# Kernel optimization log

Measured on AMD Instinct MI355X. Metric: run time of the kernel, lower is better.

Reference implementation:

```python
import jax, jax.numpy as jnp
import numpy as np

N_EMBD = 1024
N_HEAD = 16
B, T = 2, 2048
EPS_LN = 1e-5
EPS_RENORM = 1e-8


def _layernorm(x, w, b):
    mu = jnp.mean(x, axis=-1, keepdims=True)
    var = jnp.mean(jnp.square(x - mu), axis=-1, keepdims=True)
    return (x - mu) * jax.lax.rsqrt(var + EPS_LN) * w + b


def setup_inputs() -> dict:
    key = jax.random.key(0)
    ks = jax.random.split(key, 8)
    C = N_EMBD
    s = 0.02
    return {
        "x": jax.random.normal(ks[0], (B, T, C), jnp.float32),
        "ln1_w": jnp.ones((C,), jnp.float32),
        "ln1_b": jnp.zeros((C,), jnp.float32),
        "w_attn": jax.random.normal(ks[1], (C, 3 * C), jnp.float32) * s,
        "b_attn": jnp.zeros((3 * C,), jnp.float32),
        "w_attn_proj": jax.random.normal(ks[2], (C, C), jnp.float32) * s,
        "b_attn_proj": jnp.zeros((C,), jnp.float32),
        "threshold": jnp.full((N_HEAD,), 0.01, jnp.float32),
        "leak": jnp.full((N_HEAD,), 2.0, jnp.float32),
        "steepness": jnp.full((N_HEAD,), 2.0, jnp.float32),
        "ln2_w": jnp.ones((C,), jnp.float32),
        "ln2_b": jnp.zeros((C,), jnp.float32),
        "w_fc": jax.random.normal(ks[3], (C, 4 * C), jnp.float32) * s,
        "b_fc": jnp.zeros((4 * C,), jnp.float32),
        "w_mlp_proj": jax.random.normal(ks[4], (4 * C, C), jnp.float32) * s,
        "b_mlp_proj": jnp.zeros((C,), jnp.float32),
    }


def _ember_block(x, ln1_w, ln1_b, w_attn, b_attn, w_attn_proj, b_attn_proj,
                 threshold, leak, steepness, ln2_w, ln2_b,
                 w_fc, b_fc, w_mlp_proj, b_mlp_proj):
    Bx, Tx, C = x.shape
    H = N_HEAD
    D = C // H

    h = _layernorm(x, ln1_w, ln1_b)
    qkv = h @ w_attn + b_attn                      # [B,T,3C]
    q, k, v = jnp.split(qkv, 3, axis=-1)
    q = q.reshape(Bx, Tx, H, D).transpose(0, 2, 1, 3)  # [B,H,T,D]
    k = k.reshape(Bx, Tx, H, D).transpose(0, 2, 1, 3)
    v = v.reshape(Bx, Tx, H, D).transpose(0, 2, 1, 3)

    att = jnp.einsum('bhqd,bhkd->bhqk', q, k) * (1.0 / np.sqrt(D))
    causal = jnp.tril(jnp.ones((Tx, Tx), bool))
    att = jnp.where(causal[None, None], att, -jnp.inf)
    p = jax.nn.softmax(att, axis=-1)               # [B,H,T,T]

    # per-head LIF gating
    th = (jnp.abs(threshold) * 0.1)[None, :, None, None]
    lk = jax.nn.sigmoid(leak)[None, :, None, None]
    st = jax.nn.softplus(steepness)[None, :, None, None]
    fire = jax.nn.sigmoid(st * (p - th))
    w = fire + lk * (1.0 - fire)
    m = p * w
    m = m / (jnp.sum(m, axis=-1, keepdims=True) + EPS_RENORM)

    y = jnp.einsum('bhqk,bhkd->bhqd', m, v)
    y = y.transpose(0, 2, 1, 3).reshape(Bx, Tx, C)
    y = y @ w_attn_proj + b_attn_proj
    x = x + y

    h2 = _layernorm(x, ln2_w, ln2_b)
    h2 = jax.nn.gelu(h2 @ w_fc + b_fc, approximate=False)
    x = x + (h2 @ w_mlp_proj + b_mlp_proj)
    return x


def reference(x, ln1_w, ln1_b, w_attn, b_attn, w_attn_proj, b_attn_proj,
              threshold, leak, steepness, ln2_w, ln2_b,
              w_fc, b_fc, w_mlp_proj, b_mlp_proj):
    return _ember_block(x, ln1_w, ln1_b, w_attn, b_attn, w_attn_proj, b_attn_proj,
                        threshold, leak, steepness, ln2_w, ln2_b,
                        w_fc, b_fc, w_mlp_proj, b_mlp_proj)
```

## Files before the change

### kernel.cpp

```cpp
#include <hip/hip_runtime.h>
#include <hip/hip_bf16.h>
#include <math.h>

typedef __bf16 bf16_t;
typedef __bf16 bf16x8 __attribute__((ext_vector_type(8)));
typedef __bf16 bf16x4 __attribute__((ext_vector_type(4)));
typedef float  f32x4  __attribute__((ext_vector_type(4)));
typedef unsigned int u32;

static constexpr int C_    = 1024;
static constexpr int NH    = 16;
static constexpr int DH    = 64;
static constexpr int BB    = 2;
static constexpr int TT    = 2048;
static constexpr int MROWS = BB * TT;
static constexpr float LOG2E = 1.4426950408889634f;

__device__ __forceinline__ void gload_lds16(const bf16_t* src, bf16_t* dst) {
  __builtin_amdgcn_global_load_lds(
      (const __attribute__((address_space(1))) u32*)(src),
      (__attribute__((address_space(3))) u32*)(dst),
      16, 0, 0);
}

__device__ __forceinline__ u32 cvt_pk_bf16(float a, float b) {
  u32 r;
  asm("v_cvt_pk_bf16_f32 %0, %1, %2" : "=v"(r) : "v"(a), "v"(b));
  return r;
}

__device__ __forceinline__ float fexp2(float x) {
#if __has_builtin(__builtin_amdgcn_exp2f)
  return __builtin_amdgcn_exp2f(x);
#else
  return exp2f(x);
#endif
}
__device__ __forceinline__ float frcp(float x) {
#if __has_builtin(__builtin_amdgcn_rcpf)
  return __builtin_amdgcn_rcpf(x);
#else
  return 1.0f / x;
#endif
}

__device__ __forceinline__ int sc_to_t(int s, int c) {
  if (s < 32)  return s;
  if (s < 64)  return 32 + (s - 32) * 2 + c;
  if (s < 96)  return 96 + (s - 64) * 3 + c;
  return 192 + (s - 96) * 4 + c;
}

__device__ __forceinline__ void item64_to_uc(int item, int& u, int& c) {
  if (item < 8)       { u = item;               c = 0; }
  else if (item < 24) { int v = item - 8;  u = 8  + (v >> 1); c = v & 1; }
  else if (item < 48) { int v = item - 24; u = 16 + v / 3;    c = v - 3 * (v / 3); }
  else                { int v = item - 48; u = 24 + (v >> 2); c = v & 3; }
}

__global__ __launch_bounds__(256) void ln_bf16(
    const float* __restrict__ x, const float* __restrict__ w,
    const float* __restrict__ b, bf16_t* __restrict__ out)
{
  const int row = blockIdx.x;
  const int tid = threadIdx.x;
  const float4 v = reinterpret_cast<const float4*>(x + (size_t)row * C_)[tid];
  float s  = v.x + v.y + v.z + v.w;
  float s2 = v.x*v.x + v.y*v.y + v.z*v.z + v.w*v.w;
#pragma unroll
  for (int m = 1; m < 64; m <<= 1) { s += __shfl_xor(s, m); s2 += __shfl_xor(s2, m); }
  __shared__ float red[8];
  const int wv = tid >> 6;
  if ((tid & 63) == 0) { red[wv] = s; red[4 + wv] = s2; }
  __syncthreads();
  s  = red[0] + red[1] + red[2] + red[3];
  s2 = red[4] + red[5] + red[6] + red[7];
  const float mu   = s * (1.0f / C_);
  const float rstd = rsqrtf(s2 * (1.0f / C_) - mu * mu + 1e-5f);
  const float4 wv4 = reinterpret_cast<const float4*>(w)[tid];
  const float4 bv4 = reinterpret_cast<const float4*>(b)[tid];
  bf16x4 o;
  o[0] = (bf16_t)((v.x - mu) * rstd * wv4.x + bv4.x);
  o[1] = (bf16_t)((v.y - mu) * rstd * wv4.y + bv4.y);
  o[2] = (bf16_t)((v.z - mu) * rstd * wv4.z + bv4.z);
  o[3] = (bf16_t)((v.w - mu) * rstd * wv4.w + bv4.w);
  *reinterpret_cast<bf16x4*>(out + (size_t)row * C_ + tid * 4) = o;
}

__global__ __launch_bounds__(256) void ln2_fuse(
    const float* __restrict__ p0, const bf16_t* __restrict__ p1,
    const float* __restrict__ xin, const float* __restrict__ pbias,
    const float* __restrict__ w, const float* __restrict__ b,
    float* __restrict__ x2out, bf16_t* __restrict__ out)
{
  const int row = blockIdx.x;
  const int tid = threadIdx.x;
  const size_t base = (size_t)row * C_ + tid * 4;
  const float4 v0 = *reinterpret_cast<const float4*>(p0 + base);
  const bf16x4 v1 = *reinterpret_cast<const bf16x4*>(p1 + base);
  const float4 xr = *reinterpret_cast<const float4*>(xin + base);
  const float4 pb = *reinterpret_cast<const float4*>(pbias + tid * 4);
  float4 v;
  v.x = v0.x + (float)v1[0] + pb.x + xr.x;
  v.y = v0.y + (float)v1[1] + pb.y + xr.y;
  v.z = v0.z + (float)v1[2] + pb.z + xr.z;
  v.w = v0.w + (float)v1[3] + pb.w + xr.w;
  *reinterpret_cast<float4*>(x2out + base) = v;

  float s  = v.x + v.y + v.z + v.w;
  float s2 = v.x*v.x + v.y*v.y + v.z*v.z + v.w*v.w;
#pragma unroll
  for (int m = 1; m < 64; m <<= 1) { s += __shfl_xor(s, m); s2 += __shfl_xor(s2, m); }
  __shared__ float red[8];
  const int wv = tid >> 6;
  if ((tid & 63) == 0) { red[wv] = s; red[4 + wv] = s2; }
  __syncthreads();
  s  = red[0] + red[1] + red[2] + red[3];
  s2 = red[4] + red[5] + red[6] + red[7];
  const float mu   = s * (1.0f / C_);
  const float rstd = rsqrtf(s2 * (1.0f / C_) - mu * mu + 1e-5f);
  const float4 wv4 = reinterpret_cast<const float4*>(w)[tid];
  const float4 bv4 = reinterpret_cast<const float4*>(b)[tid];
  bf16x4 o;
  o[0] = (bf16_t)((v.x - mu) * rstd * wv4.x + bv4.x);
  o[1] = (bf16_t)((v.y - mu) * rstd * wv4.y + bv4.y);
  o[2] = (bf16_t)((v.z - mu) * rstd * wv4.z + bv4.z);
  o[3] = (bf16_t)((v.w - mu) * rstd * wv4.w + bv4.w);
  *reinterpret_cast<bf16x4*>(out + base) = o;
}

__global__ __launch_bounds__(256) void combine3(
    float* __restrict__ out, const bf16_t* __restrict__ p1,
    const bf16_t* __restrict__ p2, const bf16_t* __restrict__ p3,
    const float* __restrict__ bias, const float* __restrict__ resid)
{
  const size_t idx = ((size_t)blockIdx.x * 256 + threadIdx.x) * 4;
  float4 o = *reinterpret_cast<const float4*>(out + idx);
  const bf16x4 a = *reinterpret_cast<const bf16x4*>(p1 + idx);
  const bf16x4 b = *reinterpret_cast<const bf16x4*>(p2 + idx);
  const bf16x4 c = *reinterpret_cast<const bf16x4*>(p3 + idx);
  const float4 r = *reinterpret_cast<const float4*>(resid + idx);
  const int col = (int)(idx & (C_ - 1));
  const float4 bv = *reinterpret_cast<const float4*>(bias + col);
  o.x += (float)a[0] + (float)b[0] + (float)c[0] + bv.x + r.x;
  o.y += (float)a[1] + (float)b[1] + (float)c[1] + bv.y + r.y;
  o.z += (float)a[2] + (float)b[2] + (float)c[2] + bv.z + r.z;
  o.w += (float)a[3] + (float)b[3] + (float)c[3] + bv.w + r.w;
  *reinterpret_cast<float4*>(out + idx) = o;
}

__global__ __launch_bounds__(256) void transpose_w(
    const float* __restrict__ in, bf16_t* __restrict__ out, int K, int N)
{
  __shared__ float tile[32][33];
  const int tx = threadIdx.x & 31, ty = threadIdx.x >> 5;
  const int n0 = blockIdx.x * 32, k0 = blockIdx.y * 32;
#pragma unroll
  for (int i = 0; i < 4; ++i)
    tile[ty + i * 8][tx] = in[(size_t)(k0 + ty + i * 8) * N + n0 + tx];
  __syncthreads();
#pragma unroll
  for (int i = 0; i < 4; ++i)
    out[(size_t)(n0 + ty + i * 8) * K + k0 + tx] = (bf16_t)tile[tx][ty + i * 8];
}

__global__ __launch_bounds__(256) void transpose_v(
    const bf16_t* __restrict__ in, bf16_t* __restrict__ out)
{
  __shared__ bf16_t tile[32][33];
  const int bh = blockIdx.z;
  const bf16_t* src = in  + (size_t)bh * TT * DH;
  bf16_t*       dst = out + (size_t)bh * TT * DH;
  const int tx = threadIdx.x & 31, ty = threadIdx.x >> 5;
  const int t0 = blockIdx.x * 32, d0 = blockIdx.y * 32;
#pragma unroll
  for (int i = 0; i < 4; ++i)
    tile[ty + i * 8][tx] = src[(size_t)(t0 + ty + i * 8) * DH + d0 + tx];
  __syncthreads();
#pragma unroll
  for (int i = 0; i < 4; ++i)
    dst[(size_t)(d0 + ty + i * 8) * TT + t0 + tx] = tile[tx][ty + i * 8];
}

template<int EPI>
__global__ __launch_bounds__(512, 1) void gemmP(
    const bf16_t* __restrict__ A, const bf16_t* __restrict__ Bt,
    const float* __restrict__ bias, float* __restrict__ fout,
    bf16_t* __restrict__ bout0, bf16_t* __restrict__ bout1,
    bf16_t* __restrict__ bout2, int N, int Kc, int Kfull, int nbn)
{
  __shared__ bf16_t As[3][256 * 64];
  __shared__ bf16_t Bs[3][128 * 64];
  const int tid  = threadIdx.x;
  const int wave = tid >> 6, lane = tid & 63;
  const int r = lane & 15, g = lane >> 4;
  const int wm = wave >> 2, wn = wave & 3;

  const int cpx = gridDim.x >> 3;
  const int swz = (blockIdx.x & 7) * cpx + (blockIdx.x >> 3);
  const int bm = swz / nbn, bn = swz - bm * nbn;
  const int z  = blockIdx.z;
  const int k0 = z * Kc;

  const bf16_t* Abase = A  + (size_t)bm * 256 * Kfull + k0;
  const bf16_t* Bbase = Bt + (size_t)bn * 128 * Kfull + k0;

  f32x4 acc[8][2] = {};

  auto STAGE_A = [&](int buf, int kt, int pass) {
    const int idx = pass * 512 + tid;
    const int rr = idx >> 3, cc = idx & 7, gs = cc ^ (rr & 7);
    gload_lds16(Abase + (size_t)rr * Kfull + kt + gs * 8, &As[buf][idx * 8]);
  };
  auto STAGE_B = [&](int buf, int kt, int pass) {
    const int idx = pass * 512 + tid;
    const int rr = idx >> 3, cc = idx & 7, gs = cc ^ (rr & 7);
    gload_lds16(Bbase + (size_t)rr * Kfull + kt + gs * 8, &Bs[buf][idx * 8]);
  };
  auto STAGE6 = [&](int buf, int kt) {
    STAGE_A(buf, kt, 0); STAGE_A(buf, kt, 1);
    STAGE_A(buf, kt, 2); STAGE_A(buf, kt, 3);
    STAGE_B(buf, kt, 0); STAGE_B(buf, kt, 1);
  };

  const int NT = Kc >> 6;
  STAGE6(0, 0);
  STAGE6(1, 64);

  for (int t = 0; t < NT; ++t) {
    const int buf = t % 3;
    if (t + 1 < NT) asm volatile("s_waitcnt vmcnt(6)" ::: "memory");
    else            asm volatile("s_waitcnt vmcnt(0)" ::: "memory");
    __builtin_amdgcn_s_barrier();
    asm volatile("" ::: "memory");

    const bool pre = (t + 2 < NT);
    const int kn   = (t + 2) << 6;
    const int bnx  = (t + 2) % 3;

    bf16x8 bfr[2][2];
#pragma unroll
    for (int s2 = 0; s2 < 2; ++s2)
#pragma unroll
      for (int ni = 0; ni < 2; ++ni) {
        const int rr = wn * 32 + ni * 16 + r;
        bfr[s2][ni] = *reinterpret_cast<const bf16x8*>(
            &Bs[buf][rr * 64 + (((s2 << 2) | g) ^ (rr & 7)) * 8]);
      }
#pragma unroll
    for (int mh = 0; mh < 2; ++mh) {
      bf16x8 af[2][4];
#pragma unroll
      for (int s2 = 0; s2 < 2; ++s2)
#pragma unroll
        for (int mi = 0; mi < 4; ++mi) {
          const int rr = wm * 128 + (mh * 4 + mi) * 16 + r;
          af[s2][mi] = *reinterpret_cast<const bf16x8*>(
              &As[buf][rr * 64 + (((s2 << 2) | g) ^ (rr & 7)) * 8]);
        }
      if (pre) {
        if (mh == 0) { STAGE_A(bnx, kn, 0); STAGE_A(bnx, kn, 1); STAGE_A(bnx, kn, 2); }
        else         { STAGE_A(bnx, kn, 3); STAGE_B(bnx, kn, 0); STAGE_B(bnx, kn, 1); }
      }
      __builtin_amdgcn_s_setprio(1);
#pragma unroll
      for (int s2 = 0; s2 < 2; ++s2)
#pragma unroll
        for (int mi = 0; mi < 4; ++mi)
#pragma unroll
          for (int ni = 0; ni < 2; ++ni)
            acc[mh * 4 + mi][ni] = __builtin_amdgcn_mfma_f32_16x16x32_bf16(
                af[s2][mi], bfr[s2][ni], acc[mh * 4 + mi][ni], 0, 0, 0);
      __builtin_amdgcn_s_setprio(0);
    }
  }

#pragma unroll
  for (int mi = 0; mi < 8; ++mi) {
#pragma unroll
    for (int ni = 0; ni < 2; ++ni) {
      const int grow0 = bm * 256 + wm * 128 + mi * 16 + g * 4;
      const int gcol  = bn * 128 + wn * 32 + ni * 16 + r;
      const float bv = (EPI == 3) ? 0.f : bias[gcol];
#pragma unroll
      for (int i = 0; i < 4; ++i) {
        const int grow = grow0 + i;
        const float v = acc[mi][ni][i] + bv;
        if constexpr (EPI == 0) {
          const int which = gcol >> 10;
          const int c0 = gcol & 1023;
          const int hh = c0 >> 6, dd = c0 & 63;
          const int bb = grow >> 11, tt = grow & 2047;
          bf16_t* dst = (which == 0) ? bout0 : (which == 1) ? bout1 : bout2;
          dst[((size_t)(bb * NH + hh) * TT + tt) * DH + dd] = (bf16_t)v;
        } else if constexpr (EPI == 2) {
          const float gl = 0.5f * v * (1.0f + erff(v * 0.70710678118654752f));
          bout0[(size_t)grow * N + gcol] = (bf16_t)gl;
        } else {
          const size_t o = (size_t)grow * N + gcol;
          if (z == 0) fout[o] = v;
          else {
            bf16_t* pb = (z == 1) ? bout0 : (z == 2) ? bout1 : bout2;
            pb[o] = (bf16_t)v;
          }
        }
      }
    }
  }
}


__global__ __launch_bounds__(256, 4) void attn_p1(
    const bf16_t* __restrict__ Q, const bf16_t* __restrict__ Km,
    float2* __restrict__ mzP)
{
  __shared__ bf16_t Ks[2][64 * 64];
  const int tid = threadIdx.x;
  const int w = tid >> 6, lane = tid & 63;
  const int r = lane & 15, g = lane >> 4;
  const int bid = blockIdx.x;
  const int bh  = (bid & 7) * 4 + ((bid >> 3) & 3);
  int u, c; item64_to_uc(bid >> 5, u, c);
  const int cmax = u >> 3;
  const bool diag = (c == cmax);
  const int nt = diag ? (u & 7) + 1 : 8;
  const int s = 4 * u + w;
  const int row0 = u * 64 + w * 16;
  const int qrow = row0 + r;

  const bf16_t* Qh = Q  + (size_t)bh * TT * DH;
  const bf16_t* Kh = Km + (size_t)bh * TT * DH;
  const float SCL = 0.125f * LOG2E;

  bf16x8 qf[2];
#pragma unroll
  for (int s2 = 0; s2 < 2; ++s2) {
    bf16x8 t = *reinterpret_cast<const bf16x8*>(Qh + (size_t)qrow * DH + s2 * 32 + g * 8);
#pragma unroll
    for (int i = 0; i < 8; ++i) t[i] = (bf16_t)((float)t[i] * SCL);
    qf[s2] = t;
  }

  auto STAGEK = [&](int b, int t8) {
#pragma unroll
    for (int it = 0; it < 2; ++it) {
      const int idx = it * 256 + tid;
      const int rr = idx >> 3, cc = idx & 7, gs = cc ^ (rr & 7);
      gload_lds16(Kh + (size_t)(c * 512 + t8 * 64 + rr) * DH + gs * 8, &Ks[b][idx * 8]);
    }
  };

  float runM = -1e30f, runZ = 0.f;
  STAGEK(0, 0);
  for (int t8 = 0; t8 < nt; ++t8) {
    const int b = t8 & 1;
    asm volatile("s_waitcnt vmcnt(0)" ::: "memory");
    __syncthreads();
    if (t8 + 1 < nt) STAGEK(b ^ 1, t8 + 1);
    f32x4 sfT[4] = {};
#pragma unroll
    for (int s2 = 0; s2 < 2; ++s2) {
      bf16x8 kf[4];
#pragma unroll
      for (int ni = 0; ni < 4; ++ni)
        kf[ni] = *reinterpret_cast<const bf16x8*>(
            &Ks[b][(ni * 16 + r) * 64 + (((s2 << 2) | g) ^ (r & 7)) * 8]);
#pragma unroll
      for (int ni = 0; ni < 4; ++ni)
        sfT[ni] = __builtin_amdgcn_mfma_f32_16x16x32_bf16(kf[ni], qf[s2], sfT[ni], 0, 0, 0);
    }
    const bool dm = diag && (t8 == nt - 1);
    const int kbase = c * 512 + t8 * 64;
    float xv[16];
#pragma unroll
    for (int ni = 0; ni < 4; ++ni)
#pragma unroll
      for (int j = 0; j < 4; ++j) {
        float x = sfT[ni][j];
        if (dm) {
          const int kcol = kbase + ni * 16 + g * 4 + j;
          if (kcol > qrow) x = -1e30f;
        }
        xv[ni * 4 + j] = x;
      }
    float nm = runM;
#pragma unroll
    for (int e = 0; e < 16; ++e) nm = fmaxf(nm, xv[e]);
    float z = runZ * fexp2(runM - nm);
#pragma unroll
    for (int e = 0; e < 16; ++e) z += fexp2(xv[e] - nm);
    runM = nm; runZ = z;
  }
#pragma unroll
  for (int msk = 16; msk < 64; msk <<= 1) {
    const float om = __shfl_xor(runM, msk), oz = __shfl_xor(runZ, msk);
    const float nm = fmaxf(runM, om);
    runZ = runZ * fexp2(runM - nm) + oz * fexp2(om - nm);
    runM = nm;
  }
  if (lane < 16)
    mzP[((size_t)(bh * 128 + s) * 4 + c) * 16 + r] = make_float2(runM, runZ);
}

__global__ __launch_bounds__(256, 4) void attn_p3(
    const bf16_t* __restrict__ Q, const bf16_t* __restrict__ Km,
    const bf16_t* __restrict__ Vt, const float2* __restrict__ mzP,
    bf16_t* __restrict__ Y, uint2* __restrict__ yaccA,
    uint2* __restrict__ yaccB, float* __restrict__ denP,
    const float* __restrict__ thrp, const float* __restrict__ leakp,
    const float* __restrict__ steepp)
{
  __shared__ bf16_t Ks[2][64 * 64];
  __shared__ bf16_t Vs[2][64 * 64];
  __shared__ __align__(16) u32 Ms[4][512];

  const int tid = threadIdx.x;
  const int w = tid >> 6, lane = tid & 63;
  const int r = lane & 15, g = lane >> 4;
  const int bid = blockIdx.x;
  const int bh  = (bid & 7) * 4 + ((bid >> 3) & 3);
  int u, c; item64_to_uc(bid >> 5, u, c);
  const int cmax = u >> 3;
  const bool diag = (c == cmax);
  const int nt = diag ? (u & 7) + 1 : 8;
  const int nch = cmax + 1;
  const int s = 4 * u + w;
  const int row0 = u * 64 + w * 16;
  const int qrow = row0 + r;
  const int hh = bh & (NH - 1), bb = bh >> 4;

  const bf16_t* Qh  = Q  + (size_t)bh * TT * DH;
  const bf16_t* Kh  = Km + (size_t)bh * TT * DH;
  const bf16_t* Vth = Vt + (size_t)bh * TT * DH;

  const float lk  = 1.0f / (1.0f + expf(-leakp[hh]));
  const float ilk = 1.0f - lk;
  const float st  = log1pf(expf(steepp[hh]));
  const float Lst = LOG2E * st;
  const float A0  = Lst * (fabsf(thrp[hh]) * 0.1f);

  float M = -1e30f, Z = 0.f;
  for (int c2 = 0; c2 < nch; ++c2) {
    const float2 mz = mzP[((size_t)(bh * 128 + s) * 4 + c2) * 16 + r];
    const float nm = fmaxf(M, mz.x);
    Z = Z * fexp2(M - nm) + mz.y * fexp2(mz.x - nm);
    M = nm;
  }
  const float rcpZ = frcp(Z);

  const float SCL = 0.125f * LOG2E;
  bf16x8 qf[2];
#pragma unroll
  for (int s2 = 0; s2 < 2; ++s2) {
    bf16x8 t = *reinterpret_cast<const bf16x8*>(Qh + (size_t)qrow * DH + s2 * 32 + g * 8);
#pragma unroll
    for (int i = 0; i < 8; ++i) t[i] = (bf16_t)((float)t[i] * SCL);
    qf[s2] = t;
  }
  bf16x8 ones;
#pragma unroll
  for (int i = 0; i < 8; ++i) ones[i] = (bf16_t)1.0f;

  uint2* MsU2 = reinterpret_cast<uint2*>(&Ms[w][0]);
  uint4* MsU4 = reinterpret_cast<uint4*>(&Ms[w][0]);

  auto STAGE = [&](int b, int t8) {
    const int kbase = c * 512 + t8 * 64;
#pragma unroll
    for (int it = 0; it < 2; ++it) {
      const int idx = it * 256 + tid;
      const int rr = idx >> 3, cc = idx & 7, gs = cc ^ (rr & 7);
      gload_lds16(Kh + (size_t)(kbase + rr) * DH + gs * 8, &Ks[b][idx * 8]);
      gload_lds16(Vth + (size_t)rr * TT + kbase + gs * 8, &Vs[b][idx * 8]);
    }
  };

  f32x4 yacc[4] = {};
  f32x4 dacc = {};

  STAGE(0, 0);
  for (int t8 = 0; t8 < nt; ++t8) {
    const int b = t8 & 1;
    asm volatile("s_waitcnt vmcnt(0)" ::: "memory");
    __syncthreads();
    if (t8 + 1 < nt) STAGE(b ^ 1, t8 + 1);
    const int kbase = c * 512 + t8 * 64;
    f32x4 sfT[4] = {};
#pragma unroll
    for (int s2 = 0; s2 < 2; ++s2) {
      bf16x8 kf[4];
#pragma unroll
      for (int ni = 0; ni < 4; ++ni)
        kf[ni] = *reinterpret_cast<const bf16x8*>(
            &Ks[b][(ni * 16 + r) * 64 + (((s2 << 2) | g) ^ (r & 7)) * 8]);
#pragma unroll
      for (int ni = 0; ni < 4; ++ni)
        sfT[ni] = __builtin_amdgcn_mfma_f32_16x16x32_bf16(kf[ni], qf[s2], sfT[ni], 0, 0, 0);
    }
    const bool dm = diag && (t8 == nt - 1);
#pragma unroll
    for (int ni = 0; ni < 4; ++ni) {
      float mv[4];
#pragma unroll
      for (int j = 0; j < 4; ++j) {
        float x = sfT[ni][j];
        if (dm) {
          const int kcol = kbase + ni * 16 + g * 4 + j;
          if (kcol > qrow) x = -1e30f;
        }
        const float p    = fexp2(x - M) * rcpZ;
        const float fire = frcp(1.0f + fexp2(A0 - Lst * p));
        mv[j] = p * fmaf(ilk, fire, lk);
      }
      MsU2[r * 16 + ((4 * ni + g) ^ ((r & 7) << 1))] =
          make_uint2(cvt_pk_bf16(mv[0], mv[1]), cvt_pk_bf16(mv[2], mv[3]));
    }
#pragma unroll
    for (int s2 = 0; s2 < 2; ++s2) {
      const uint4 aw = MsU4[r * 8 + ((s2 * 4 + g) ^ (r & 7))];
      const bf16x8 af = __builtin_bit_cast(bf16x8, aw);
      bf16x8 vf[4];
#pragma unroll
      for (int ni = 0; ni < 4; ++ni)
        vf[ni] = *reinterpret_cast<const bf16x8*>(
            &Vs[b][(ni * 16 + r) * 64 + (((s2 << 2) | g) ^ (r & 7)) * 8]);
#pragma unroll
      for (int ni = 0; ni < 4; ++ni)
        yacc[ni] = __builtin_amdgcn_mfma_f32_16x16x32_bf16(af, vf[ni], yacc[ni], 0, 0, 0);
      dacc = __builtin_amdgcn_mfma_f32_16x16x32_bf16(af, ones, dacc, 0, 0, 0);
    }
  }

  if (nch == 1) {
#pragma unroll
    for (int j = 0; j < 4; ++j) {
      const float rd = frcp(dacc[j] + 1e-8f);
      const int t = row0 + g * 4 + j;
#pragma unroll
      for (int ni = 0; ni < 4; ++ni)
        Y[((size_t)(bb * TT + t)) * C_ + hh * DH + ni * 16 + r] =
            (bf16_t)(yacc[ni][j] * rd);
    }
  } else {
    const int pid = bh * 288 + (sc_to_t(s, c) - 32);
    uint2* pb = (pid < 4096) ? (yaccA + (size_t)pid * 256)
                             : (yaccB + (size_t)(pid - 4096) * 256);
#pragma unroll
    for (int ni = 0; ni < 4; ++ni)
      pb[ni * 64 + lane] =
          make_uint2(cvt_pk_bf16(yacc[ni][0], yacc[ni][1]),
                     cvt_pk_bf16(yacc[ni][2], yacc[ni][3]));
    if (r == 0)
      *reinterpret_cast<float4*>(&denP[(size_t)pid * 16 + g * 4]) =
          make_float4(dacc[0], dacc[1], dacc[2], dacc[3]);
  }
}

__global__ __launch_bounds__(256) void attn_p4(
    const uint2* __restrict__ yaccA, const uint2* __restrict__ yaccB,
    const float* __restrict__ denP, bf16_t* __restrict__ Y)
{
  const int bid = blockIdx.x;
  const int bh  = bid / 96;
  const int s   = 32 + (bid - bh * 96);
  const int nch = (s >> 5) + 1;
  const int hh = bh & (NH - 1), bb = bh >> 4;

  const int tid = threadIdx.x;
  const int w = tid >> 6, lane = tid & 63;
  const int r = lane & 15, g = lane >> 4;

  float acc[4] = {};
  float den[4] = {};
  for (int c = 0; c < nch; ++c) {
    const int pid = bh * 288 + (sc_to_t(s, c) - 32);
    const uint2* pb = (pid < 4096) ? (yaccA + (size_t)pid * 256)
                                   : (yaccB + (size_t)(pid - 4096) * 256);
    const uint2 u = pb[w * 64 + lane];
    acc[0] += __builtin_bit_cast(float, (u.x & 0xFFFFu) << 16);
    acc[1] += __builtin_bit_cast(float, (u.x & 0xFFFF0000u));
    acc[2] += __builtin_bit_cast(float, (u.y & 0xFFFFu) << 16);
    acc[3] += __builtin_bit_cast(float, (u.y & 0xFFFF0000u));
    const float4 d4 = *reinterpret_cast<const float4*>(&denP[(size_t)pid * 16 + g * 4]);
    den[0] += d4.x; den[1] += d4.y; den[2] += d4.z; den[3] += d4.w;
  }
#pragma unroll
  for (int j = 0; j < 4; ++j) {
    const float rd = 1.0f / (den[j] + 1e-8f);
    const int t = s * 16 + g * 4 + j;
    Y[((size_t)(bb * TT + t)) * C_ + hh * DH + w * 16 + r] = (bf16_t)(acc[j] * rd);
  }
}

extern "C" void kernel_launch(void* const* d_in, const int* in_sizes, int n_in,
                              void* d_out, int out_size, void* d_ws, size_t ws_size,
                              hipStream_t stream)
{
  const float* x      = (const float*)d_in[0];
  const float* ln1_w  = (const float*)d_in[1];
  const float* ln1_b  = (const float*)d_in[2];
  const float* w_attn = (const float*)d_in[3];
  const float* b_attn = (const float*)d_in[4];
  const float* w_proj = (const float*)d_in[5];
  const float* b_proj = (const float*)d_in[6];
  const float* thr    = (const float*)d_in[7];
  const float* leak   = (const float*)d_in[8];
  const float* steep  = (const float*)d_in[9];
  const float* ln2_w  = (const float*)d_in[10];
  const float* ln2_b  = (const float*)d_in[11];
  const float* w_fc   = (const float*)d_in[12];
  const float* b_fc   = (const float*)d_in[13];
  const float* w_mlp  = (const float*)d_in[14];
  const float* b_mlp  = (const float*)d_in[15];

  char* ws = (char*)d_ws;
  bf16_t* q    = (bf16_t*)(ws + 0);
  bf16_t* k    = (bf16_t*)(ws + 8388608);
  bf16_t* v    = (bf16_t*)(ws + 16777216);
  bf16_t* vT   = (bf16_t*)(ws + 25165824);
  bf16_t* gbuf = (bf16_t*)(ws + 0);
  bf16_t* hbuf = (bf16_t*)(ws + 33554432);
  float*  x2   = (float*) (ws + 41943040);
  bf16_t* wT_attn = (bf16_t*)(ws + 58720256);
  bf16_t* wT_proj = (bf16_t*)(ws + 65011712);
  bf16_t* wT_fc   = (bf16_t*)(ws + 67108864);
  bf16_t* wT_mlp  = (bf16_t*)(ws + 75497472);

  uint2* yaccA = (uint2*)(ws + 16777216);
  uint2* yaccB = (uint2*)(ws + 41943040);
  float* denP  = (float*)(ws + 52428800);
  float2* mzP  = (float2*)(ws + 53477376);

  bf16_t* pp1 = (bf16_t*)(ws + 0);
  bf16_t* mp1 = (bf16_t*)(ws + 33554432);
  bf16_t* mp2 = (bf16_t*)(ws + 58720256);
  bf16_t* mp3 = (bf16_t*)(ws + 67108864);

  float* out = (float*)d_out;

  ln_bf16<<<dim3(MROWS), dim3(256), 0, stream>>>(x, ln1_w, ln1_b, hbuf);
  transpose_w<<<dim3(96, 32),  dim3(256), 0, stream>>>(w_attn, wT_attn, 1024, 3072);
  transpose_w<<<dim3(32, 32),  dim3(256), 0, stream>>>(w_proj, wT_proj, 1024, 1024);
  transpose_w<<<dim3(128, 32), dim3(256), 0, stream>>>(w_fc,   wT_fc,   1024, 4096);
  transpose_w<<<dim3(32, 128), dim3(256), 0, stream>>>(w_mlp,  wT_mlp,  4096, 1024);

  gemmP<0><<<dim3(384, 1, 1), dim3(512), 0, stream>>>(
      hbuf, wT_attn, b_attn, nullptr, q, k, v, 3072, 1024, 1024, 24);
  transpose_v<<<dim3(64, 2, 32), dim3(256), 0, stream>>>(v, vT);

  attn_p1<<<dim3(2560), dim3(256), 0, stream>>>(q, k, mzP);
  attn_p3<<<dim3(2560), dim3(256), 0, stream>>>(
      q, k, vT, mzP, hbuf, yaccA, yaccB, denP, thr, leak, steep);
  attn_p4<<<dim3(3072), dim3(256), 0, stream>>>(yaccA, yaccB, denP, hbuf);

  gemmP<3><<<dim3(128, 1, 2), dim3(512), 0, stream>>>(
      hbuf, wT_proj, nullptr, x2, pp1, nullptr, nullptr, 1024, 512, 1024, 8);

  ln2_fuse<<<dim3(MROWS), dim3(256), 0, stream>>>(
      x2, pp1, x, b_proj, ln2_w, ln2_b, x2, hbuf);

  gemmP<2><<<dim3(512, 1, 1), dim3(512), 0, stream>>>(
      hbuf, wT_fc, b_fc, nullptr, gbuf, nullptr, nullptr, 4096, 1024, 1024, 32);

  gemmP<3><<<dim3(128, 1, 4), dim3(512), 0, stream>>>(
      gbuf, wT_mlp, nullptr, out, mp1, mp2, mp3, 1024, 1024, 4096, 8);

  combine3<<<dim3(4096), dim3(256), 0, stream>>>(out, mp1, mp2, mp3, b_mlp, x2);
}
```

Before: 292.9 us.

## Fuse V transpose into QKV epilogue, widen attention blocks, add split-K GEMM

The QKV GEMM epilogue now writes V directly in transposed layout, which removes the separate transpose_v kernel. Both attention kernels move from 256-thread to 512-thread blocks covering 128 query rows, with a new work-item mapping, half the grid, and causal masking applied on every tile of a diagonal chunk. The projection and MLP-down GEMMs move to a new simpler single-buffered 128x128 split-K kernel with more blocks. The risks are scattered, uncoalesced stores for V in the epilogue, lost pipelining in the new GEMM, and extra masking work.

After: 309.4 us. 1.06x slower.

```diff
diff --git a/kernel.cpp b/kernel.cpp
--- a/kernel.cpp
+++ b/kernel.cpp
@@ -51,11 +51,11 @@
   return 192 + (s - 96) * 4 + c;
 }
 
-__device__ __forceinline__ void item64_to_uc(int item, int& u, int& c) {
-  if (item < 8)       { u = item;               c = 0; }
-  else if (item < 24) { int v = item - 8;  u = 8  + (v >> 1); c = v & 1; }
-  else if (item < 48) { int v = item - 24; u = 16 + v / 3;    c = v - 3 * (v / 3); }
-  else                { int v = item - 48; u = 24 + (v >> 2); c = v & 3; }
+__device__ __forceinline__ void item40_to_uc(int t, int& u, int& c) {
+  if (t < 4)       { u = t;                c = 0; }
+  else if (t < 12) { int v = t - 4;  u = 4  + (v >> 1); c = v & 1; }
+  else if (t < 24) { int v = t - 12; u = 8  + v / 3;    c = v - 3 * (v / 3); }
+  else             { int v = t - 24; u = 12 + (v >> 2); c = v & 3; }
 }
 
 __global__ __launch_bounds__(256) void ln_bf16(
@@ -164,24 +164,6 @@
     out[(size_t)(n0 + ty + i * 8) * K + k0 + tx] = (bf16_t)tile[tx][ty + i * 8];
 }
 
-__global__ __launch_bounds__(256) void transpose_v(
-    const bf16_t* __restrict__ in, bf16_t* __restrict__ out)
-{
-  __shared__ bf16_t tile[32][33];
-  const int bh = blockIdx.z;
-  const bf16_t* src = in  + (size_t)bh * TT * DH;
-  bf16_t*       dst = out + (size_t)bh * TT * DH;
-  const int tx = threadIdx.x & 31, ty = threadIdx.x >> 5;
-  const int t0 = blockIdx.x * 32, d0 = blockIdx.y * 32;
-#pragma unroll
-  for (int i = 0; i < 4; ++i)
-    tile[ty + i * 8][tx] = src[(size_t)(t0 + ty + i * 8) * DH + d0 + tx];
-  __syncthreads();
-#pragma unroll
-  for (int i = 0; i < 4; ++i)
-    dst[(size_t)(d0 + ty + i * 8) * TT + t0 + tx] = tile[tx][ty + i * 8];
-}
-
 template<int EPI>
 __global__ __launch_bounds__(512, 1) void gemmP(
     const bf16_t* __restrict__ A, const bf16_t* __restrict__ Bt,
@@ -207,20 +189,20 @@
 
   f32x4 acc[8][2] = {};
 
-  auto STAGE_A = [&](int buf, int kt, int pass) {
+  auto STG_A = [&](int buf, int kt, int pass) {
     const int idx = pass * 512 + tid;
     const int rr = idx >> 3, cc = idx & 7, gs = cc ^ (rr & 7);
     gload_lds16(Abase + (size_t)rr * Kfull + kt + gs * 8, &As[buf][idx * 8]);
   };
-  auto STAGE_B = [&](int buf, int kt, int pass) {
+  auto STG_B = [&](int buf, int kt, int pass) {
     const int idx = pass * 512 + tid;
     const int rr = idx >> 3, cc = idx & 7, gs = cc ^ (rr & 7);
     gload_lds16(Bbase + (size_t)rr * Kfull + kt + gs * 8, &Bs[buf][idx * 8]);
   };
   auto STAGE6 = [&](int buf, int kt) {
-    STAGE_A(buf, kt, 0); STAGE_A(buf, kt, 1);
-    STAGE_A(buf, kt, 2); STAGE_A(buf, kt, 3);
-    STAGE_B(buf, kt, 0); STAGE_B(buf, kt, 1);
+    STG_A(buf, kt, 0); STG_A(buf, kt, 1);
+    STG_A(buf, kt, 2); STG_A(buf, kt, 3);
+    STG_B(buf, kt, 0); STG_B(buf, kt, 1);
   };
 
   const int NT = Kc >> 6;
@@ -259,8 +241,8 @@
               &As[buf][rr * 64 + (((s2 << 2) | g) ^ (rr & 7)) * 8]);
         }
       if (pre) {
-        if (mh == 0) { STAGE_A(bnx, kn, 0); STAGE_A(bnx, kn, 1); STAGE_A(bnx, kn, 2); }
-        else         { STAGE_A(bnx, kn, 3); STAGE_B(bnx, kn, 0); STAGE_B(bnx, kn, 1); }
+        if (mh == 0) { STG_A(bnx, kn, 0); STG_A(bnx, kn, 1); STG_A(bnx, kn, 2); }
+        else         { STG_A(bnx, kn, 3); STG_B(bnx, kn, 0); STG_B(bnx, kn, 1); }
       }
       __builtin_amdgcn_s_setprio(1);
 #pragma unroll
@@ -281,7 +263,7 @@
     for (int ni = 0; ni < 2; ++ni) {
       const int grow0 = bm * 256 + wm * 128 + mi * 16 + g * 4;
       const int gcol  = bn * 128 + wn * 32 + ni * 16 + r;
-      const float bv = (EPI == 3) ? 0.f : bias[gcol];
+      const float bv = bias[gcol];
 #pragma unroll
       for (int i = 0; i < 4; ++i) {
         const int grow = grow0 + i;
@@ -291,26 +273,110 @@
           const int c0 = gcol & 1023;
           const int hh = c0 >> 6, dd = c0 & 63;
           const int bb = grow >> 11, tt = grow & 2047;
-          bf16_t* dst = (which == 0) ? bout0 : (which == 1) ? bout1 : bout2;
-          dst[((size_t)(bb * NH + hh) * TT + tt) * DH + dd] = (bf16_t)v;
-        } else if constexpr (EPI == 2) {
+          if (which == 2)
+            bout2[((size_t)(bb * NH + hh) * DH + dd) * TT + tt] = (bf16_t)v;
+          else {
+            bf16_t* dst = (which == 0) ? bout0 : bout1;
+            dst[((size_t)(bb * NH + hh) * TT + tt) * DH + dd] = (bf16_t)v;
+          }
+        } else {
           const float gl = 0.5f * v * (1.0f + erff(v * 0.70710678118654752f));
           bout0[(size_t)grow * N + gcol] = (bf16_t)gl;
-        } else {
-          const size_t o = (size_t)grow * N + gcol;
-          if (z == 0) fout[o] = v;
-          else {
-            bf16_t* pb = (z == 1) ? bout0 : (z == 2) ? bout1 : bout2;
-            pb[o] = (bf16_t)v;
-          }
         }
       }
     }
   }
 }
 
-
-__global__ __launch_bounds__(256, 4) void attn_p1(
+__global__ __launch_bounds__(256) void gemm_sk(
+    const bf16_t* __restrict__ A, const bf16_t* __restrict__ Bt,
+    float* __restrict__ fout, bf16_t* __restrict__ bout0,
+    bf16_t* __restrict__ bout1, bf16_t* __restrict__ bout2,
+    int M, int N, int Kc, int Kfull)
+{
+  constexpr int BM = 128, BN = 128, BK = 64;
+  __shared__ bf16_t As[BM * BK];
+  __shared__ bf16_t Bs[BN * BK];
+  const int tid  = threadIdx.x;
+  const int wave = tid >> 6, lane = tid & 63;
+  const int r = lane & 15, g = lane >> 4;
+  const int wm = wave >> 1, wn = wave & 1;
+  const int bm = blockIdx.x, bn = blockIdx.y;
+  const int z  = blockIdx.z;
+  const int kstart = z * Kc;
+
+  const bf16_t* Abase = A  + (size_t)bm * BM * Kfull;
+  const bf16_t* Bbase = Bt + (size_t)bn * BN * Kfull;
+
+  f32x4 acc[4][4] = {};
+
+  for (int kt = kstart; kt < kstart + Kc; kt += BK) {
+#pragma unroll
+    for (int it = 0; it < 4; ++it) {
+      const int c0 = it * 256 + wave * 64;
+      const int idx = c0 + lane;
+      const int rr = idx >> 3, cc = idx & 7;
+      const int gs = cc ^ (rr & 7);
+      gload_lds16(Abase + (size_t)rr * Kfull + kt + gs * 8, As + c0 * 8);
+    }
+#pragma unroll
+    for (int it = 0; it < 4; ++it) {
+      const int c0 = it * 256 + wave * 64;
+      const int idx = c0 + lane;
+      const int rr = idx >> 3, cc = idx & 7;
+      const int gs = cc ^ (rr & 7);
+      gload_lds16(Bbase + (size_t)rr * Kfull + kt + gs * 8, Bs + c0 * 8);
+    }
+    asm volatile("s_waitcnt vmcnt(0)" ::: "memory");
+    __syncthreads();
+#pragma unroll
+    for (int s = 0; s < 2; ++s) {
+      bf16x8 af[4], bfr[4];
+#pragma unroll
+      for (int mi = 0; mi < 4; ++mi) {
+        const int rr = wm * 64 + mi * 16 + r;
+        const int ch = (s * 4 + g) ^ (rr & 7);
+        af[mi] = *reinterpret_cast<const bf16x8*>(&As[rr * BK + ch * 8]);
+      }
+#pragma unroll
+      for (int ni = 0; ni < 4; ++ni) {
+        const int rr = wn * 64 + ni * 16 + r;
+        const int ch = (s * 4 + g) ^ (rr & 7);
+        bfr[ni] = *reinterpret_cast<const bf16x8*>(&Bs[rr * BK + ch * 8]);
+      }
+#pragma unroll
+      for (int mi = 0; mi < 4; ++mi)
+#pragma unroll
+        for (int ni = 0; ni < 4; ++ni)
+          acc[mi][ni] = __builtin_amdgcn_mfma_f32_16x16x32_bf16(
+              af[mi], bfr[ni], acc[mi][ni], 0, 0, 0);
+    }
+    __syncthreads();
+  }
+
+#pragma unroll
+  for (int mi = 0; mi < 4; ++mi) {
+#pragma unroll
+    for (int ni = 0; ni < 4; ++ni) {
+      const int grow0 = bm * BM + wm * 64 + mi * 16 + g * 4;
+      const int gcol  = bn * BN + wn * 64 + ni * 16 + r;
+#pragma unroll
+      for (int i = 0; i < 4; ++i) {
+        const int grow = grow0 + i;
+        const float v = acc[mi][ni][i];
+        const size_t o = (size_t)grow * N + gcol;
+        if (z == 0) fout[o] = v;
+        else {
+          bf16_t* pb = (z == 1) ? bout0 : (z == 2) ? bout1 : bout2;
+          pb[o] = (bf16_t)v;
+        }
+      }
+    }
+  }
+}
+
+
+__global__ __launch_bounds__(512, 4) void attn_p1(
     const bf16_t* __restrict__ Q, const bf16_t* __restrict__ Km,
     float2* __restrict__ mzP)
 {
@@ -320,13 +386,12 @@
   const int r = lane & 15, g = lane >> 4;
   const int bid = blockIdx.x;
   const int bh  = (bid & 7) * 4 + ((bid >> 3) & 3);
-  int u, c; item64_to_uc(bid >> 5, u, c);
-  const int cmax = u >> 3;
+  int gu, c; item40_to_uc(bid >> 5, gu, c);
+  const int cmax = gu >> 2;
   const bool diag = (c == cmax);
-  const int nt = diag ? (u & 7) + 1 : 8;
-  const int s = 4 * u + w;
-  const int row0 = u * 64 + w * 16;
-  const int qrow = row0 + r;
+  const int nt = diag ? ((gu & 3) * 2 + 2) : 8;
+  const int s = gu * 8 + w;
+  const int qrow = gu * 128 + w * 16 + r;
 
   const bf16_t* Qh = Q  + (size_t)bh * TT * DH;
   const bf16_t* Kh = Km + (size_t)bh * TT * DH;
@@ -342,12 +407,8 @@
   }
 
   auto STAGEK = [&](int b, int t8) {
-#pragma unroll
-    for (int it = 0; it < 2; ++it) {
-      const int idx = it * 256 + tid;
-      const int rr = idx >> 3, cc = idx & 7, gs = cc ^ (rr & 7);
-      gload_lds16(Kh + (size_t)(c * 512 + t8 * 64 + rr) * DH + gs * 8, &Ks[b][idx * 8]);
-    }
+    const int rr = tid >> 3, cc = tid & 7, gs = cc ^ (rr & 7);
+    gload_lds16(Kh + (size_t)(c * 512 + t8 * 64 + rr) * DH + gs * 8, &Ks[b][tid * 8]);
   };
 
   float runM = -1e30f, runZ = 0.f;
@@ -369,7 +430,6 @@
       for (int ni = 0; ni < 4; ++ni)
         sfT[ni] = __builtin_amdgcn_mfma_f32_16x16x32_bf16(kf[ni], qf[s2], sfT[ni], 0, 0, 0);
     }
-    const bool dm = diag && (t8 == nt - 1);
     const int kbase = c * 512 + t8 * 64;
     float xv[16];
 #pragma unroll
@@ -377,7 +437,7 @@
 #pragma unroll
       for (int j = 0; j < 4; ++j) {
         float x = sfT[ni][j];
-        if (dm) {
+        if (diag) {
           const int kcol = kbase + ni * 16 + g * 4 + j;
           if (kcol > qrow) x = -1e30f;
         }
@@ -402,7 +462,7 @@
     mzP[((size_t)(bh * 128 + s) * 4 + c) * 16 + r] = make_float2(runM, runZ);
 }
 
-__global__ __launch_bounds__(256, 4) void attn_p3(
+__global__ __launch_bounds__(512, 2) void attn_p3(
     const bf16_t* __restrict__ Q, const bf16_t* __restrict__ Km,
     const bf16_t* __restrict__ Vt, const float2* __restrict__ mzP,
     bf16_t* __restrict__ Y, uint2* __restrict__ yaccA,
@@ -412,21 +472,21 @@
 {
   __shared__ bf16_t Ks[2][64 * 64];
   __shared__ bf16_t Vs[2][64 * 64];
-  __shared__ __align__(16) u32 Ms[4][512];
+  __shared__ __align__(16) u32 Ms[8][512];
 
   const int tid = threadIdx.x;
   const int w = tid >> 6, lane = tid & 63;
   const int r = lane & 15, g = lane >> 4;
   const int bid = blockIdx.x;
   const int bh  = (bid & 7) * 4 + ((bid >> 3) & 3);
-  int u, c; item64_to_uc(bid >> 5, u, c);
-  const int cmax = u >> 3;
+  int gu, c; item40_to_uc(bid >> 5, gu, c);
+  const int cmax = gu >> 2;
   const bool diag = (c == cmax);
-  const int nt = diag ? (u & 7) + 1 : 8;
+  const int nt = diag ? ((gu & 3) * 2 + 2) : 8;
   const int nch = cmax + 1;
-  const int s = 4 * u + w;
-  const int row0 = u * 64 + w * 16;
-  const int qrow = row0 + r;
+  const int s = gu * 8 + w;
+  const int row0w = gu * 128 + w * 16;
+  const int qrow = row0w + r;
   const int hh = bh & (NH - 1), bb = bh >> 4;
 
   const bf16_t* Qh  = Q  + (size_t)bh * TT * DH;
@@ -466,13 +526,9 @@
 
   auto STAGE = [&](int b, int t8) {
     const int kbase = c * 512 + t8 * 64;
-#pragma unroll
-    for (int it = 0; it < 2; ++it) {
-      const int idx = it * 256 + tid;
-      const int rr = idx >> 3, cc = idx & 7, gs = cc ^ (rr & 7);
-      gload_lds16(Kh + (size_t)(kbase + rr) * DH + gs * 8, &Ks[b][idx * 8]);
-      gload_lds16(Vth + (size_t)rr * TT + kbase + gs * 8, &Vs[b][idx * 8]);
-    }
+    const int rr = tid >> 3, cc = tid & 7, gs = cc ^ (rr & 7);
+    gload_lds16(Kh + (size_t)(kbase + rr) * DH + gs * 8, &Ks[b][tid * 8]);
+    gload_lds16(Vth + (size_t)rr * TT + kbase + gs * 8, &Vs[b][tid * 8]);
   };
 
   f32x4 yacc[4] = {};
@@ -497,14 +553,13 @@
       for (int ni = 0; ni < 4; ++ni)
         sfT[ni] = __builtin_amdgcn_mfma_f32_16x16x32_bf16(kf[ni], qf[s2], sfT[ni], 0, 0, 0);
     }
-    const bool dm = diag && (t8 == nt - 1);
 #pragma unroll
     for (int ni = 0; ni < 4; ++ni) {
       float mv[4];
 #pragma unroll
       for (int j = 0; j < 4; ++j) {
         float x = sfT[ni][j];
-        if (dm) {
+        if (diag) {
           const int kcol = kbase + ni * 16 + g * 4 + j;
           if (kcol > qrow) x = -1e30f;
         }
@@ -535,7 +590,7 @@
 #pragma unroll
     for (int j = 0; j < 4; ++j) {
       const float rd = frcp(dacc[j] + 1e-8f);
-      const int t = row0 + g * 4 + j;
+      const int t = row0w + g * 4 + j;
 #pragma unroll
       for (int ni = 0; ni < 4; ++ni)
         Y[((size_t)(bb * TT + t)) * C_ + hh * DH + ni * 16 + r] =
@@ -616,7 +671,6 @@
   char* ws = (char*)d_ws;
   bf16_t* q    = (bf16_t*)(ws + 0);
   bf16_t* k    = (bf16_t*)(ws + 8388608);
-  bf16_t* v    = (bf16_t*)(ws + 16777216);
   bf16_t* vT   = (bf16_t*)(ws + 25165824);
   bf16_t* gbuf = (bf16_t*)(ws + 0);
   bf16_t* hbuf = (bf16_t*)(ws + 33554432);
@@ -645,16 +699,15 @@
   transpose_w<<<dim3(32, 128), dim3(256), 0, stream>>>(w_mlp,  wT_mlp,  4096, 1024);
 
   gemmP<0><<<dim3(384, 1, 1), dim3(512), 0, stream>>>(
-      hbuf, wT_attn, b_attn, nullptr, q, k, v, 3072, 1024, 1024, 24);
-  transpose_v<<<dim3(64, 2, 32), dim3(256), 0, stream>>>(v, vT);
-
-  attn_p1<<<dim3(2560), dim3(256), 0, stream>>>(q, k, mzP);
-  attn_p3<<<dim3(2560), dim3(256), 0, stream>>>(
+      hbuf, wT_attn, b_attn, nullptr, q, k, vT, 3072, 1024, 1024, 24);
+
+  attn_p1<<<dim3(1280), dim3(512), 0, stream>>>(q, k, mzP);
+  attn_p3<<<dim3(1280), dim3(512), 0, stream>>>(
       q, k, vT, mzP, hbuf, yaccA, yaccB, denP, thr, leak, steep);
   attn_p4<<<dim3(3072), dim3(256), 0, stream>>>(yaccA, yaccB, denP, hbuf);
 
-  gemmP<3><<<dim3(128, 1, 2), dim3(512), 0, stream>>>(
-      hbuf, wT_proj, nullptr, x2, pp1, nullptr, nullptr, 1024, 512, 1024, 8);
+  gemm_sk<<<dim3(32, 8, 2), dim3(256), 0, stream>>>(
+      hbuf, wT_proj, x2, pp1, nullptr, nullptr, MROWS, 1024, 512, 1024);
 
   ln2_fuse<<<dim3(MROWS), dim3(256), 0, stream>>>(
       x2, pp1, x, b_proj, ln2_w, ln2_b, x2, hbuf);
@@ -662,8 +715,8 @@
   gemmP<2><<<dim3(512, 1, 1), dim3(512), 0, stream>>>(
       hbuf, wT_fc, b_fc, nullptr, gbuf, nullptr, nullptr, 4096, 1024, 1024, 32);
 
-  gemmP<3><<<dim3(128, 1, 4), dim3(512), 0, stream>>>(
-      gbuf, wT_mlp, nullptr, out, mp1, mp2, mp3, 1024, 1024, 4096, 8);
+  gemm_sk<<<dim3(32, 8, 4), dim3(256), 0, stream>>>(
+      gbuf, wT_mlp, out, mp1, mp2, mp3, MROWS, 1024, 1024, 4096);
 
   combine3<<<dim3(4096), dim3(256), 0, stream>>>(out, mp1, mp2, mp3, b_mlp, x2);
 }
```
